# Performance work log

Measured on AMD Instinct MI355X. Metric: run time of the kernel, lower is better.

## Reference

```python
import jax, jax.numpy as jnp
import numpy as np

B, H, S, D = 2, 16, 2048, 64


def setup_inputs() -> dict:
    key = jax.random.key(0)
    kq, kk, kv = jax.random.split(key, 3)
    queries = jax.random.normal(kq, (B, H, S, D), dtype=jnp.float32)
    keys = jax.random.normal(kk, (B, H, S, D), dtype=jnp.float32)
    values = jax.random.normal(kv, (B, H, S, D), dtype=jnp.float32)
    # causal mask: True = attend, False = masked (matches masked_fill(mask == 0, -inf))
    mask = jnp.tril(jnp.ones((S, S), dtype=bool))[None, None, :, :]
    return {"queries": queries, "keys": keys, "values": values, "mask": mask}


def reference(queries, keys, values, mask):
    d_k = queries.shape[-1]
    scale = 1.0 / jnp.sqrt(jnp.asarray(d_k, dtype=queries.dtype))
    # scores: [B,H,S,S]
    scores = jnp.einsum("bhqd,bhkd->bhqk", queries, keys) * scale
    scores = jnp.where(mask, scores, -jnp.inf)
    attention = jax.nn.softmax(scores, axis=-1)
    # dropout p=0.0 (eval-mode reference) -> identity
    return jnp.einsum("bhqk,bhkd->bhqd", attention, values)
```

## Files before the change

kernel.cpp:

```cpp
#include <hip/hip_runtime.h>
#include <hip/hip_bf16.h>

#define S_LEN 2048
#define D_DIM 64
#define KVB   64
#define QS    (0.125f * 1.44269504088896341f)

using f32x4  = __attribute__((ext_vector_type(4))) float;
using bf16x8 = __attribute__((ext_vector_type(8))) short;

__device__ __forceinline__ unsigned short f2bf(float f) {
    return __builtin_bit_cast(unsigned short, __float2bfloat16(f));
}
__device__ __forceinline__ unsigned pk2bf(float lo, float hi) {
    return (unsigned)f2bf(lo) | ((unsigned)f2bf(hi) << 16);
}
__device__ __forceinline__ int swz(int r, int c) {
    return (r * 64 + c) ^ ((r & 7) << 3);
}

template<int C>
__device__ __forceinline__ float dppf(float x) {
    return __builtin_bit_cast(float,
        __builtin_amdgcn_mov_dpp(__builtin_bit_cast(int, x), C, 0xf, 0xf, true));
}
__device__ __forceinline__ float red16_max(float v) {
    v = fmaxf(v, dppf<0xB1>(v));
    v = fmaxf(v, dppf<0x4E>(v));
    v = fmaxf(v, dppf<0x141>(v));
    v = fmaxf(v, dppf<0x140>(v));
    return v;
}
__device__ __forceinline__ float red16_sum(float v) {
    v += dppf<0xB1>(v);
    v += dppf<0x4E>(v);
    v += dppf<0x141>(v);
    v += dppf<0x140>(v);
    return v;
}

typedef const __attribute__((address_space(1))) unsigned short* gas_p;
typedef __attribute__((address_space(3))) unsigned short*       las_p;
__device__ __forceinline__ void stage16(const unsigned short* g, unsigned short* l) {
    __builtin_amdgcn_global_load_lds((gas_p)g, (las_p)l, 16, 0, 0);
}

__global__ __launch_bounds__(256)
void prep_k(const float* __restrict__ Kg, unsigned short* __restrict__ wsK) {
    const int base = (blockIdx.x * 256 + threadIdx.x) * 8;
    const int bh   = base >> 17;
    const int rem  = base & 131071;
    const int r    = rem >> 6;
    const int c0   = rem & 63;
    f32x4 a = *(const f32x4*)(Kg + base);
    f32x4 b = *(const f32x4*)(Kg + base + 4);
    union { uint4 w4; unsigned u[4]; } w;
    w.u[0] = pk2bf(a[0], a[1]); w.u[1] = pk2bf(a[2], a[3]);
    w.u[2] = pk2bf(b[0], b[1]); w.u[3] = pk2bf(b[2], b[3]);
    *(uint4*)&wsK[bh * 131072 + (r >> 6) * 4096 + swz(r & 63, c0)] = w.w4;
}

__global__ __launch_bounds__(256)
void prep_v(const float* __restrict__ Vg, unsigned short* __restrict__ wsV) {
    __shared__ float ldsF[64 * 68];
    const int bh  = blockIdx.x >> 5;
    const int t   = blockIdx.x & 31;
    const int tid = threadIdx.x;
    const int kvr = tid >> 2;
    const int c0  = (tid & 3) << 4;
    const float* src = Vg + (size_t)bh * 131072 + (size_t)(t * 64 + kvr) * 64 + c0;
    #pragma unroll
    for (int j = 0; j < 4; ++j)
        *(f32x4*)&ldsF[kvr * 68 + c0 + j * 4] = *(const f32x4*)(src + j * 4);
    __syncthreads();
    #pragma unroll
    for (int i = 0; i < 2; ++i) {
        const int d   = tid & 63;
        const int kv0 = ((tid >> 6) << 3) + (i << 5);
        float p[8];
        #pragma unroll
        for (int j = 0; j < 8; ++j) p[j] = ldsF[(kv0 + j) * 68 + d];
        union { uint4 w4; unsigned u[4]; } w;
        w.u[0] = pk2bf(p[0], p[1]); w.u[1] = pk2bf(p[2], p[3]);
        w.u[2] = pk2bf(p[4], p[5]); w.u[3] = pk2bf(p[6], p[7]);
        *(uint4*)&wsV[bh * 131072 + t * 4096 + swz(d, kv0)] = w.w4;
    }
}

__global__ __launch_bounds__(256, 4)
void attn_fast(const float* __restrict__ Qg, const unsigned short* __restrict__ wsK,
               const unsigned short* __restrict__ wsV, float* __restrict__ Og) {
    __shared__ __align__(16) unsigned short lds[20480];

    const int wg = blockIdx.x;
    const int x  = wg & 7;
    const int s  = (wg >> 3) & 31;
    const int r  = wg >> 8;
    const int bh = x * 4 + r;
    const int q  = (r & 1) ? (31 - s) : s;

    const int tid  = threadIdx.x;
    const int wid  = tid >> 6;
    const int lane = tid & 63;
    const int lo   = lane & 15;
    const int hi   = lane >> 4;

    const float* Qp = Qg + (size_t)bh * (S_LEN * D_DIM);
    float*       Op = Og + (size_t)bh * (S_LEN * D_DIM);
    const unsigned short* kws = wsK + (size_t)bh * 131072;
    const unsigned short* vws = wsV + (size_t)bh * 131072;

    const int qrow0 = q * 64 + wid * 16;

    bf16x8 qf[2];
    #pragma unroll
    for (int kc = 0; kc < 2; ++kc) {
        const float* src = Qp + (size_t)(qrow0 + lo) * D_DIM + kc * 32 + hi * 8;
        f32x4 a = *(const f32x4*)src;
        f32x4 b = *(const f32x4*)(src + 4);
        union { bf16x8 v; unsigned u[4]; } fr;
        fr.u[0] = pk2bf(a[0] * QS, a[1] * QS);
        fr.u[1] = pk2bf(a[2] * QS, a[3] * QS);
        fr.u[2] = pk2bf(b[0] * QS, b[1] * QS);
        fr.u[3] = pk2bf(b[2] * QS, b[3] * QS);
        qf[kc] = fr.v;
    }

    float mrow[4], lrow[4];
    f32x4 oacc[4];
    #pragma unroll
    for (int rr = 0; rr < 4; ++rr) { mrow[rr] = -INFINITY; lrow[rr] = 0.f; }
    #pragma unroll
    for (int dn = 0; dn < 4; ++dn) oacc[dn] = f32x4{0.f, 0.f, 0.f, 0.f};

    const int pbase = 16384 + (wid << 10);
    const int T = q + 1;

    #pragma unroll
    for (int j = 0; j < 2; ++j) {
        const int so = (wid * 2 + j) * 512;
        stage16(kws + so + lane * 8, &lds[so]);
        stage16(vws + so + lane * 8, &lds[4096 + so]);
    }
    __syncthreads();

    for (int t = 0; t < T; ++t) {
        const int kA = (t & 1) << 13;
        const int vA = kA + 4096;
        const bool pf = (t + 1 < T);

        if (pf) {
            const int nA = ((t + 1) & 1) << 13;
            const int tb = (t + 1) * 4096;
            #pragma unroll
            for (int j = 0; j < 2; ++j) {
                const int so = (wid * 2 + j) * 512;
                stage16(kws + tb + so + lane * 8, &lds[nA + so]);
                stage16(vws + tb + so + lane * 8, &lds[nA + 4096 + so]);
            }
        }

        f32x4 sc[4];
        __builtin_amdgcn_s_setprio(1);
        #pragma unroll
        for (int nt = 0; nt < 4; ++nt) {
            f32x4 acc = f32x4{0.f, 0.f, 0.f, 0.f};
            #pragma unroll
            for (int kc = 0; kc < 2; ++kc) {
                bf16x8 kf = *(const bf16x8*)&lds[kA + swz(nt * 16 + lo, kc * 32 + hi * 8)];
                acc = __builtin_amdgcn_mfma_f32_16x16x32_bf16(qf[kc], kf, acc, 0, 0, 0);
            }
            sc[nt] = acc;
        }
        __builtin_amdgcn_s_setprio(0);
        if (t == q) {
            const int kb = t * KVB;
            #pragma unroll
            for (int nt = 0; nt < 4; ++nt)
                #pragma unroll
                for (int rr = 0; rr < 4; ++rr)
                    if (kb + nt * 16 + lo > qrow0 + hi * 4 + rr) sc[nt][rr] = -INFINITY;
        }
        float pm[4];
        #pragma unroll
        for (int rr = 0; rr < 4; ++rr)
            pm[rr] = red16_max(fmaxf(fmaxf(sc[0][rr], sc[1][rr]), fmaxf(sc[2][rr], sc[3][rr])));

        bool resc = false;
        #pragma unroll
        for (int rr = 0; rr < 4; ++rr) resc |= (pm[rr] > mrow[rr] + 8.f);
        if (__any(resc)) {
            #pragma unroll
            for (int rr = 0; rr < 4; ++rr) {
                const float mn = fmaxf(mrow[rr], pm[rr]);
                const float al = __builtin_amdgcn_exp2f(mrow[rr] - mn);
                mrow[rr] = mn;
                lrow[rr] *= al;
                #pragma unroll
                for (int dn = 0; dn < 4; ++dn) oacc[dn][rr] *= al;
            }
        }
        float rs[4] = {0.f, 0.f, 0.f, 0.f};
        #pragma unroll
        for (int nt = 0; nt < 4; ++nt)
            #pragma unroll
            for (int rr = 0; rr < 4; ++rr) {
                float p = __builtin_amdgcn_exp2f(sc[nt][rr] - mrow[rr]);
                rs[rr] += p;
                lds[pbase + swz(hi * 4 + rr, nt * 16 + lo)] = f2bf(p);
            }
        #pragma unroll
        for (int rr = 0; rr < 4; ++rr) lrow[rr] += red16_sum(rs[rr]);

        __builtin_amdgcn_s_setprio(1);
        #pragma unroll
        for (int dn = 0; dn < 4; ++dn)
            #pragma unroll
            for (int kc = 0; kc < 2; ++kc) {
                bf16x8 pfr = *(const bf16x8*)&lds[pbase + swz(lo, kc * 32 + hi * 8)];
                bf16x8 vfr = *(const bf16x8*)&lds[vA + swz(dn * 16 + lo, kc * 32 + hi * 8)];
                oacc[dn] = __builtin_amdgcn_mfma_f32_16x16x32_bf16(pfr, vfr, oacc[dn], 0, 0, 0);
            }
        __builtin_amdgcn_s_setprio(0);

        __syncthreads();
    }

    #pragma unroll
    for (int rr = 0; rr < 4; ++rr) {
        const float inv = 1.0f / lrow[rr];
        #pragma unroll
        for (int dn = 0; dn < 4; ++dn)
            Op[(size_t)(qrow0 + hi * 4 + rr) * D_DIM + dn * 16 + lo] = oacc[dn][rr] * inv;
    }
}

__global__ __launch_bounds__(256, 4)
void attn_fb(const float* __restrict__ Qg, const float* __restrict__ Kg,
             const float* __restrict__ Vg, float* __restrict__ Og) {
    __shared__ __align__(16) unsigned short lds[20480];
    const int wg = blockIdx.x;
    const int x  = wg & 7;
    const int s  = (wg >> 3) & 31;
    const int r  = wg >> 8;
    const int bh = x * 4 + r;
    const int q  = (r & 1) ? (31 - s) : s;
    const int tid  = threadIdx.x;
    const int wid  = tid >> 6;
    const int lane = tid & 63;
    const int lo   = lane & 15;
    const int hi   = lane >> 4;
    const size_t boff = (size_t)bh * (S_LEN * D_DIM);
    const float* Qp = Qg + boff;
    const float* Kp = Kg + boff;
    const float* Vp = Vg + boff;
    float*       Op = Og + boff;
    const int qrow0 = q * 64 + wid * 16;
    bf16x8 qf[2];
    #pragma unroll
    for (int kc = 0; kc < 2; ++kc) {
        const float* src = Qp + (size_t)(qrow0 + lo) * D_DIM + kc * 32 + hi * 8;
        f32x4 a = *(const f32x4*)src;
        f32x4 b = *(const f32x4*)(src + 4);
        union { bf16x8 v; unsigned u[4]; } fr;
        fr.u[0] = pk2bf(a[0] * QS, a[1] * QS);
        fr.u[1] = pk2bf(a[2] * QS, a[3] * QS);
        fr.u[2] = pk2bf(b[0] * QS, b[1] * QS);
        fr.u[3] = pk2bf(b[2] * QS, b[3] * QS);
        qf[kc] = fr.v;
    }
    float mrow[4], lrow[4];
    f32x4 oacc[4];
    #pragma unroll
    for (int rr = 0; rr < 4; ++rr) { mrow[rr] = -INFINITY; lrow[rr] = 0.f; }
    #pragma unroll
    for (int dn = 0; dn < 4; ++dn) oacc[dn] = f32x4{0.f, 0.f, 0.f, 0.f};
    const int kr    = tid >> 2;
    const int kcb   = (tid & 3) << 4;
    const int vr    = (tid & 31) << 1;
    const int vcb   = (tid >> 5) << 3;
    const int pbase = 16384 + (wid << 10);
    const int T = q + 1;
    f32x4 kst[4], vst[4];
    {
        const float* ks = Kp + (size_t)kr * D_DIM + kcb;
        kst[0] = *(const f32x4*)ks;       kst[1] = *(const f32x4*)(ks + 4);
        kst[2] = *(const f32x4*)(ks + 8); kst[3] = *(const f32x4*)(ks + 12);
        const float* vs = Vp + (size_t)vr * D_DIM + vcb;
        vst[0] = *(const f32x4*)vs;           vst[1] = *(const f32x4*)(vs + 4);
        vst[2] = *(const f32x4*)(vs + D_DIM); vst[3] = *(const f32x4*)(vs + D_DIM + 4);
        union { uint4 w4; unsigned u[4]; } w;
        w.u[0] = pk2bf(kst[0][0], kst[0][1]); w.u[1] = pk2bf(kst[0][2], kst[0][3]);
        w.u[2] = pk2bf(kst[1][0], kst[1][1]); w.u[3] = pk2bf(kst[1][2], kst[1][3]);
        *(uint4*)&lds[swz(kr, kcb)] = w.w4;
        w.u[0] = pk2bf(kst[2][0], kst[2][1]); w.u[1] = pk2bf(kst[2][2], kst[2][3]);
        w.u[2] = pk2bf(kst[3][0], kst[3][1]); w.u[3] = pk2bf(kst[3][2], kst[3][3]);
        *(uint4*)&lds[swz(kr, kcb + 8)] = w.w4;
        #pragma unroll
        for (int c = 0; c < 8; ++c) {
            unsigned pv = pk2bf(vst[c >> 2][c & 3], vst[2 + (c >> 2)][c & 3]);
            *(unsigned*)&lds[4096 + swz(vcb + c, vr)] = pv;
        }
    }
    __syncthreads();
    for (int t = 0; t < T; ++t) {
        const int kA = (t & 1) << 13;
        const int vA = kA + 4096;
        const bool pf = (t + 1 < T);
        if (pf) {
            const int nb = (t + 1) * KVB;
            const float* ks = Kp + (size_t)(nb + kr) * D_DIM + kcb;
            kst[0] = *(const f32x4*)ks;       kst[1] = *(const f32x4*)(ks + 4);
            kst[2] = *(const f32x4*)(ks + 8); kst[3] = *(const f32x4*)(ks + 12);
            const float* vs = Vp + (size_t)(nb + vr) * D_DIM + vcb;
            vst[0] = *(const f32x4*)vs;           vst[1] = *(const f32x4*)(vs + 4);
            vst[2] = *(const f32x4*)(vs + D_DIM); vst[3] = *(const f32x4*)(vs + D_DIM + 4);
        }
        f32x4 sc[4];
        __builtin_amdgcn_s_setprio(1);
        #pragma unroll
        for (int nt = 0; nt < 4; ++nt) {
            f32x4 acc = f32x4{0.f, 0.f, 0.f, 0.f};
            #pragma unroll
            for (int kc = 0; kc < 2; ++kc) {
                bf16x8 kf = *(const bf16x8*)&lds[kA + swz(nt * 16 + lo, kc * 32 + hi * 8)];
                acc = __builtin_amdgcn_mfma_f32_16x16x32_bf16(qf[kc], kf, acc, 0, 0, 0);
            }
            sc[nt] = acc;
        }
        __builtin_amdgcn_s_setprio(0);
        if (t == q) {
            const int kb = t * KVB;
            #pragma unroll
            for (int nt = 0; nt < 4; ++nt)
                #pragma unroll
                for (int rr = 0; rr < 4; ++rr)
                    if (kb + nt * 16 + lo > qrow0 + hi * 4 + rr) sc[nt][rr] = -INFINITY;
        }
        float pm[4];
        #pragma unroll
        for (int rr = 0; rr < 4; ++rr)
            pm[rr] = red16_max(fmaxf(fmaxf(sc[0][rr], sc[1][rr]), fmaxf(sc[2][rr], sc[3][rr])));
        bool resc = false;
        #pragma unroll
        for (int rr = 0; rr < 4; ++rr) resc |= (pm[rr] > mrow[rr] + 8.f);
        if (__any(resc)) {
            #pragma unroll
            for (int rr = 0; rr < 4; ++rr) {
                const float mn = fmaxf(mrow[rr], pm[rr]);
                const float al = __builtin_amdgcn_exp2f(mrow[rr] - mn);
                mrow[rr] = mn;
                lrow[rr] *= al;
                #pragma unroll
                for (int dn = 0; dn < 4; ++dn) oacc[dn][rr] *= al;
            }
        }
        float rs[4] = {0.f, 0.f, 0.f, 0.f};
        #pragma unroll
        for (int nt = 0; nt < 4; ++nt)
            #pragma unroll
            for (int rr = 0; rr < 4; ++rr) {
                float p = __builtin_amdgcn_exp2f(sc[nt][rr] - mrow[rr]);
                rs[rr] += p;
                lds[pbase + swz(hi * 4 + rr, nt * 16 + lo)] = f2bf(p);
            }
        #pragma unroll
        for (int rr = 0; rr < 4; ++rr) lrow[rr] += red16_sum(rs[rr]);
        __builtin_amdgcn_s_setprio(1);
        #pragma unroll
        for (int dn = 0; dn < 4; ++dn)
            #pragma unroll
            for (int kc = 0; kc < 2; ++kc) {
                bf16x8 pfr = *(const bf16x8*)&lds[pbase + swz(lo, kc * 32 + hi * 8)];
                bf16x8 vfr = *(const bf16x8*)&lds[vA + swz(dn * 16 + lo, kc * 32 + hi * 8)];
                oacc[dn] = __builtin_amdgcn_mfma_f32_16x16x32_bf16(pfr, vfr, oacc[dn], 0, 0, 0);
            }
        __builtin_amdgcn_s_setprio(0);
        if (pf) {
            const int nA = ((t + 1) & 1) << 13;
            union { uint4 w4; unsigned u[4]; } w;
            w.u[0] = pk2bf(kst[0][0], kst[0][1]); w.u[1] = pk2bf(kst[0][2], kst[0][3]);
            w.u[2] = pk2bf(kst[1][0], kst[1][1]); w.u[3] = pk2bf(kst[1][2], kst[1][3]);
            *(uint4*)&lds[nA + swz(kr, kcb)] = w.w4;
            w.u[0] = pk2bf(kst[2][0], kst[2][1]); w.u[1] = pk2bf(kst[2][2], kst[2][3]);
            w.u[2] = pk2bf(kst[3][0], kst[3][1]); w.u[3] = pk2bf(kst[3][2], kst[3][3]);
            *(uint4*)&lds[nA + swz(kr, kcb + 8)] = w.w4;
            #pragma unroll
            for (int c = 0; c < 8; ++c) {
                unsigned pv = pk2bf(vst[c >> 2][c & 3], vst[2 + (c >> 2)][c & 3]);
                *(unsigned*)&lds[nA + 4096 + swz(vcb + c, vr)] = pv;
            }
        }
        __syncthreads();
    }
    #pragma unroll
    for (int rr = 0; rr < 4; ++rr) {
        const float inv = 1.0f / lrow[rr];
        #pragma unroll
        for (int dn = 0; dn < 4; ++dn)
            Op[(size_t)(qrow0 + hi * 4 + rr) * D_DIM + dn * 16 + lo] = oacc[dn][rr] * inv;
    }
}

extern "C" void kernel_launch(void* const* d_in, const int* in_sizes, int n_in,
                              void* d_out, int out_size, void* d_ws, size_t ws_size,
                              hipStream_t stream) {
    const float* Q = (const float*)d_in[0];
    const float* K = (const float*)d_in[1];
    const float* V = (const float*)d_in[2];
    float* O = (float*)d_out;
    const size_t wsNeed = (size_t)32 * 131072 * 2 * sizeof(unsigned short);
    if (ws_size >= wsNeed) {
        unsigned short* wsK = (unsigned short*)d_ws;
        unsigned short* wsV = wsK + (size_t)32 * 131072;
        prep_k<<<dim3(2048), dim3(256), 0, stream>>>(K, wsK);
        prep_v<<<dim3(1024), dim3(256), 0, stream>>>(V, wsV);
        attn_fast<<<dim3(1024), dim3(256), 0, stream>>>(Q, wsK, wsV, O);
    } else {
        attn_fb<<<dim3(1024), dim3(256), 0, stream>>>(Q, K, V, O);
    }
}
```

Measured before the change: 151.0 us.

## Split long causal query tiles across two workgroups and merge partials

Query tiles with 16 or more KV tiles are split into two KV halves, each handled by a separate workgroup that writes unnormalized partial outputs plus row max and sum to workspace. A new combine kernel rescales and merges the two halves. This targets the tail imbalance of causal attention, where the longest tiles dominate runtime. The K and V prep kernels are also fused into one launch that writes transposed V through LDS. The cost is extra workspace traffic, a third launch, and a dependence on workspace being large enough.

Result: no change. 149.2 us (-1.2%).

```diff
diff --git a/kernel.cpp b/kernel.cpp
--- a/kernel.cpp
+++ b/kernel.cpp
@@ -46,58 +46,77 @@
 }
 
 __global__ __launch_bounds__(256)
-void prep_k(const float* __restrict__ Kg, unsigned short* __restrict__ wsK) {
-    const int base = (blockIdx.x * 256 + threadIdx.x) * 8;
-    const int bh   = base >> 17;
-    const int rem  = base & 131071;
-    const int r    = rem >> 6;
-    const int c0   = rem & 63;
-    f32x4 a = *(const f32x4*)(Kg + base);
-    f32x4 b = *(const f32x4*)(Kg + base + 4);
-    union { uint4 w4; unsigned u[4]; } w;
-    w.u[0] = pk2bf(a[0], a[1]); w.u[1] = pk2bf(a[2], a[3]);
-    w.u[2] = pk2bf(b[0], b[1]); w.u[3] = pk2bf(b[2], b[3]);
-    *(uint4*)&wsK[bh * 131072 + (r >> 6) * 4096 + swz(r & 63, c0)] = w.w4;
-}
-
-__global__ __launch_bounds__(256)
-void prep_v(const float* __restrict__ Vg, unsigned short* __restrict__ wsV) {
-    __shared__ float ldsF[64 * 68];
+void prep_kv(const float* __restrict__ Kg, const float* __restrict__ Vg,
+             unsigned short* __restrict__ wsK, unsigned short* __restrict__ wsV) {
+    __shared__ float vf[64 * 68];
+    __shared__ __align__(16) unsigned short vt[4096];
     const int bh  = blockIdx.x >> 5;
     const int t   = blockIdx.x & 31;
     const int tid = threadIdx.x;
-    const int kvr = tid >> 2;
-    const int c0  = (tid & 3) << 4;
-    const float* src = Vg + (size_t)bh * 131072 + (size_t)(t * 64 + kvr) * 64 + c0;
-    #pragma unroll
-    for (int j = 0; j < 4; ++j)
-        *(f32x4*)&ldsF[kvr * 68 + c0 + j * 4] = *(const f32x4*)(src + j * 4);
+    const size_t gbase = (size_t)bh * 131072 + (size_t)t * 4096;
+    {
+        const int e  = tid * 16;
+        const int r  = e >> 6;
+        const int c0 = e & 63;
+        const float* src = Kg + gbase + e;
+        f32x4 a = *(const f32x4*)src;
+        f32x4 b = *(const f32x4*)(src + 4);
+        f32x4 cc = *(const f32x4*)(src + 8);
+        f32x4 d = *(const f32x4*)(src + 12);
+        union { uint4 w4; unsigned u[4]; } w;
+        w.u[0] = pk2bf(a[0], a[1]);  w.u[1] = pk2bf(a[2], a[3]);
+        w.u[2] = pk2bf(b[0], b[1]);  w.u[3] = pk2bf(b[2], b[3]);
+        *(uint4*)&wsK[gbase + swz(r, c0)] = w.w4;
+        w.u[0] = pk2bf(cc[0], cc[1]); w.u[1] = pk2bf(cc[2], cc[3]);
+        w.u[2] = pk2bf(d[0], d[1]);   w.u[3] = pk2bf(d[2], d[3]);
+        *(uint4*)&wsK[gbase + swz(r, c0 + 8)] = w.w4;
+        const float* vsrc = Vg + gbase + e;
+        *(f32x4*)&vf[r * 68 + c0]      = *(const f32x4*)vsrc;
+        *(f32x4*)&vf[r * 68 + c0 + 4]  = *(const f32x4*)(vsrc + 4);
+        *(f32x4*)&vf[r * 68 + c0 + 8]  = *(const f32x4*)(vsrc + 8);
+        *(f32x4*)&vf[r * 68 + c0 + 12] = *(const f32x4*)(vsrc + 12);
+    }
     __syncthreads();
-    #pragma unroll
-    for (int i = 0; i < 2; ++i) {
+    {
         const int d   = tid & 63;
-        const int kv0 = ((tid >> 6) << 3) + (i << 5);
-        float p[8];
-        #pragma unroll
-        for (int j = 0; j < 8; ++j) p[j] = ldsF[(kv0 + j) * 68 + d];
+        const int kv0 = (tid >> 6) << 4;
+        float p[16];
+        #pragma unroll
+        for (int j = 0; j < 16; ++j) p[j] = vf[(kv0 + j) * 68 + d];
         union { uint4 w4; unsigned u[4]; } w;
-        w.u[0] = pk2bf(p[0], p[1]); w.u[1] = pk2bf(p[2], p[3]);
-        w.u[2] = pk2bf(p[4], p[5]); w.u[3] = pk2bf(p[6], p[7]);
-        *(uint4*)&wsV[bh * 131072 + t * 4096 + swz(d, kv0)] = w.w4;
+        w.u[0] = pk2bf(p[0], p[1]);   w.u[1] = pk2bf(p[2], p[3]);
+        w.u[2] = pk2bf(p[4], p[5]);   w.u[3] = pk2bf(p[6], p[7]);
+        *(uint4*)&vt[swz(d, kv0)] = w.w4;
+        w.u[0] = pk2bf(p[8], p[9]);   w.u[1] = pk2bf(p[10], p[11]);
+        w.u[2] = pk2bf(p[12], p[13]); w.u[3] = pk2bf(p[14], p[15]);
+        *(uint4*)&vt[swz(d, kv0 + 8)] = w.w4;
+    }
+    __syncthreads();
+    {
+        uint4* dst = (uint4*)&wsV[gbase];
+        const uint4* srcv = (const uint4*)vt;
+        dst[tid] = srcv[tid];
+        dst[tid + 256] = srcv[tid + 256];
     }
 }
 
 __global__ __launch_bounds__(256, 4)
-void attn_fast(const float* __restrict__ Qg, const unsigned short* __restrict__ wsK,
-               const unsigned short* __restrict__ wsV, float* __restrict__ Og) {
+void attn_sp(const float* __restrict__ Qg, const unsigned short* __restrict__ wsK,
+             const unsigned short* __restrict__ wsV, float* __restrict__ Og,
+             float* __restrict__ wsP) {
     __shared__ __align__(16) unsigned short lds[20480];
 
-    const int wg = blockIdx.x;
-    const int x  = wg & 7;
-    const int s  = (wg >> 3) & 31;
-    const int r  = wg >> 8;
-    const int bh = x * 4 + r;
-    const int q  = (r & 1) ? (31 - s) : s;
+    const int blk    = blockIdx.x;
+    const int xcd    = blk & 7;
+    const int within = blk >> 3;
+    const int w      = within >> 2;
+    const int bh     = xcd * 4 + (within & 3);
+    int q, c;
+    if (w < 32) { q = 31 - (w >> 1); c = w & 1; }
+    else        { q = 47 - w;        c = 0;     }
+    const int nc   = (q >= 16) ? 2 : 1;
+    const int t0   = (c == 0) ? 0 : 16;
+    const int tEnd = (c == 0 && q >= 16) ? 16 : (q + 1);
 
     const int tid  = threadIdx.x;
     const int wid  = tid >> 6;
@@ -134,20 +153,22 @@
     for (int dn = 0; dn < 4; ++dn) oacc[dn] = f32x4{0.f, 0.f, 0.f, 0.f};
 
     const int pbase = 16384 + (wid << 10);
-    const int T = q + 1;
-
-    #pragma unroll
-    for (int j = 0; j < 2; ++j) {
-        const int so = (wid * 2 + j) * 512;
-        stage16(kws + so + lane * 8, &lds[so]);
-        stage16(vws + so + lane * 8, &lds[4096 + so]);
+
+    {
+        const int tb = t0 * 4096;
+        #pragma unroll
+        for (int j = 0; j < 2; ++j) {
+            const int so = (wid * 2 + j) * 512;
+            stage16(kws + tb + so + lane * 8, &lds[so]);
+            stage16(vws + tb + so + lane * 8, &lds[4096 + so]);
+        }
     }
     __syncthreads();
 
-    for (int t = 0; t < T; ++t) {
+    for (int t = t0; t < tEnd; ++t) {
         const int kA = (t & 1) << 13;
         const int vA = kA + 4096;
-        const bool pf = (t + 1 < T);
+        const bool pf = (t + 1 < tEnd);
 
         if (pf) {
             const int nA = ((t + 1) & 1) << 13;
@@ -226,6 +247,186 @@
         __syncthreads();
     }
 
+    if (nc == 1) {
+        #pragma unroll
+        for (int rr = 0; rr < 4; ++rr) {
+            const float inv = 1.0f / lrow[rr];
+            #pragma unroll
+            for (int dn = 0; dn < 4; ++dn)
+                Op[(size_t)(qrow0 + hi * 4 + rr) * D_DIM + dn * 16 + lo] = oacc[dn][rr] * inv;
+        }
+    } else {
+        float* slot = wsP + (size_t)(bh * 32 + (q - 16) * 2 + c) * 4224;
+        #pragma unroll
+        for (int rr = 0; rr < 4; ++rr) {
+            const int row = wid * 16 + hi * 4 + rr;
+            #pragma unroll
+            for (int dn = 0; dn < 4; ++dn)
+                slot[row * 64 + dn * 16 + lo] = oacc[dn][rr];
+        }
+        if (lo == 0) {
+            #pragma unroll
+            for (int rr = 0; rr < 4; ++rr) {
+                const int row = wid * 16 + hi * 4 + rr;
+                slot[4096 + row] = mrow[rr];
+                slot[4160 + row] = lrow[rr];
+            }
+        }
+    }
+}
+
+__global__ __launch_bounds__(256)
+void combine_k(const float* __restrict__ wsP, float* __restrict__ Og) {
+    const int bh  = blockIdx.x >> 4;
+    const int qq  = blockIdx.x & 15;
+    const int q   = 16 + qq;
+    const int tid = threadIdx.x;
+    const int row = tid >> 2;
+    const int cg  = (tid & 3) << 4;
+    const float* s0 = wsP + (size_t)(bh * 32 + qq * 2) * 4224;
+    const float* s1 = s0 + 4224;
+    const float m0 = s0[4096 + row], l0 = s0[4160 + row];
+    const float m1 = s1[4096 + row], l1 = s1[4160 + row];
+    const float M  = fmaxf(m0, m1);
+    const float w0 = __builtin_amdgcn_exp2f(m0 - M);
+    const float w1 = __builtin_amdgcn_exp2f(m1 - M);
+    const float inv = 1.0f / (w0 * l0 + w1 * l1);
+    float* dst = Og + (size_t)bh * 131072 + (size_t)(q * 64 + row) * 64 + cg;
+    #pragma unroll
+    for (int j = 0; j < 16; j += 4) {
+        f32x4 a = *(const f32x4*)(s0 + row * 64 + cg + j);
+        f32x4 b = *(const f32x4*)(s1 + row * 64 + cg + j);
+        f32x4 o;
+        #pragma unroll
+        for (int e = 0; e < 4; ++e) o[e] = (w0 * a[e] + w1 * b[e]) * inv;
+        *(f32x4*)(dst + j) = o;
+    }
+}
+
+__global__ __launch_bounds__(256, 4)
+void attn_fast(const float* __restrict__ Qg, const unsigned short* __restrict__ wsK,
+               const unsigned short* __restrict__ wsV, float* __restrict__ Og) {
+    __shared__ __align__(16) unsigned short lds[20480];
+    const int wg = blockIdx.x;
+    const int x  = wg & 7;
+    const int s  = (wg >> 3) & 31;
+    const int r  = wg >> 8;
+    const int bh = x * 4 + r;
+    const int q  = (r & 1) ? (31 - s) : s;
+    const int tid  = threadIdx.x;
+    const int wid  = tid >> 6;
+    const int lane = tid & 63;
+    const int lo   = lane & 15;
+    const int hi   = lane >> 4;
+    const float* Qp = Qg + (size_t)bh * (S_LEN * D_DIM);
+    float*       Op = Og + (size_t)bh * (S_LEN * D_DIM);
+    const unsigned short* kws = wsK + (size_t)bh * 131072;
+    const unsigned short* vws = wsV + (size_t)bh * 131072;
+    const int qrow0 = q * 64 + wid * 16;
+    bf16x8 qf[2];
+    #pragma unroll
+    for (int kc = 0; kc < 2; ++kc) {
+        const float* src = Qp + (size_t)(qrow0 + lo) * D_DIM + kc * 32 + hi * 8;
+        f32x4 a = *(const f32x4*)src;
+        f32x4 b = *(const f32x4*)(src + 4);
+        union { bf16x8 v; unsigned u[4]; } fr;
+        fr.u[0] = pk2bf(a[0] * QS, a[1] * QS);
+        fr.u[1] = pk2bf(a[2] * QS, a[3] * QS);
+        fr.u[2] = pk2bf(b[0] * QS, b[1] * QS);
+        fr.u[3] = pk2bf(b[2] * QS, b[3] * QS);
+        qf[kc] = fr.v;
+    }
+    float mrow[4], lrow[4];
+    f32x4 oacc[4];
+    #pragma unroll
+    for (int rr = 0; rr < 4; ++rr) { mrow[rr] = -INFINITY; lrow[rr] = 0.f; }
+    #pragma unroll
+    for (int dn = 0; dn < 4; ++dn) oacc[dn] = f32x4{0.f, 0.f, 0.f, 0.f};
+    const int pbase = 16384 + (wid << 10);
+    const int T = q + 1;
+    #pragma unroll
+    for (int j = 0; j < 2; ++j) {
+        const int so = (wid * 2 + j) * 512;
+        stage16(kws + so + lane * 8, &lds[so]);
+        stage16(vws + so + lane * 8, &lds[4096 + so]);
+    }
+    __syncthreads();
+    for (int t = 0; t < T; ++t) {
+        const int kA = (t & 1) << 13;
+        const int vA = kA + 4096;
+        const bool pf = (t + 1 < T);
+        if (pf) {
+            const int nA = ((t + 1) & 1) << 13;
+            const int tb = (t + 1) * 4096;
+            #pragma unroll
+            for (int j = 0; j < 2; ++j) {
+                const int so = (wid * 2 + j) * 512;
+                stage16(kws + tb + so + lane * 8, &lds[nA + so]);
+                stage16(vws + tb + so + lane * 8, &lds[nA + 4096 + so]);
+            }
+        }
+        f32x4 sc[4];
+        __builtin_amdgcn_s_setprio(1);
+        #pragma unroll
+        for (int nt = 0; nt < 4; ++nt) {
+            f32x4 acc = f32x4{0.f, 0.f, 0.f, 0.f};
+            #pragma unroll
+            for (int kc = 0; kc < 2; ++kc) {
+                bf16x8 kf = *(const bf16x8*)&lds[kA + swz(nt * 16 + lo, kc * 32 + hi * 8)];
+                acc = __builtin_amdgcn_mfma_f32_16x16x32_bf16(qf[kc], kf, acc, 0, 0, 0);
+            }
+            sc[nt] = acc;
+        }
+        __builtin_amdgcn_s_setprio(0);
+        if (t == q) {
+            const int kb = t * KVB;
+            #pragma unroll
+            for (int nt = 0; nt < 4; ++nt)
+                #pragma unroll
+                for (int rr = 0; rr < 4; ++rr)
+                    if (kb + nt * 16 + lo > qrow0 + hi * 4 + rr) sc[nt][rr] = -INFINITY;
+        }
+        float pm[4];
+        #pragma unroll
+        for (int rr = 0; rr < 4; ++rr)
+            pm[rr] = red16_max(fmaxf(fmaxf(sc[0][rr], sc[1][rr]), fmaxf(sc[2][rr], sc[3][rr])));
+        bool resc = false;
+        #pragma unroll
+        for (int rr = 0; rr < 4; ++rr) resc |= (pm[rr] > mrow[rr] + 8.f);
+        if (__any(resc)) {
+            #pragma unroll
+            for (int rr = 0; rr < 4; ++rr) {
+                const float mn = fmaxf(mrow[rr], pm[rr]);
+                const float al = __builtin_amdgcn_exp2f(mrow[rr] - mn);
+                mrow[rr] = mn;
+                lrow[rr] *= al;
+                #pragma unroll
+                for (int dn = 0; dn < 4; ++dn) oacc[dn][rr] *= al;
+            }
+        }
+        float rs[4] = {0.f, 0.f, 0.f, 0.f};
+        #pragma unroll
+        for (int nt = 0; nt < 4; ++nt)
+            #pragma unroll
+            for (int rr = 0; rr < 4; ++rr) {
+                float p = __builtin_amdgcn_exp2f(sc[nt][rr] - mrow[rr]);
+                rs[rr] += p;
+                lds[pbase + swz(hi * 4 + rr, nt * 16 + lo)] = f2bf(p);
+            }
+        #pragma unroll
+        for (int rr = 0; rr < 4; ++rr) lrow[rr] += red16_sum(rs[rr]);
+        __builtin_amdgcn_s_setprio(1);
+        #pragma unroll
+        for (int dn = 0; dn < 4; ++dn)
+            #pragma unroll
+            for (int kc = 0; kc < 2; ++kc) {
+                bf16x8 pfr = *(const bf16x8*)&lds[pbase + swz(lo, kc * 32 + hi * 8)];
+                bf16x8 vfr = *(const bf16x8*)&lds[vA + swz(dn * 16 + lo, kc * 32 + hi * 8)];
+                oacc[dn] = __builtin_amdgcn_mfma_f32_16x16x32_bf16(pfr, vfr, oacc[dn], 0, 0, 0);
+            }
+        __builtin_amdgcn_s_setprio(0);
+        __syncthreads();
+    }
     #pragma unroll
     for (int rr = 0; rr < 4; ++rr) {
         const float inv = 1.0f / lrow[rr];
@@ -297,9 +498,9 @@
         w.u[2] = pk2bf(kst[3][0], kst[3][1]); w.u[3] = pk2bf(kst[3][2], kst[3][3]);
         *(uint4*)&lds[swz(kr, kcb + 8)] = w.w4;
         #pragma unroll
-        for (int c = 0; c < 8; ++c) {
-            unsigned pv = pk2bf(vst[c >> 2][c & 3], vst[2 + (c >> 2)][c & 3]);
-            *(unsigned*)&lds[4096 + swz(vcb + c, vr)] = pv;
+        for (int cc = 0; cc < 8; ++cc) {
+            unsigned pv = pk2bf(vst[cc >> 2][cc & 3], vst[2 + (cc >> 2)][cc & 3]);
+            *(unsigned*)&lds[4096 + swz(vcb + cc, vr)] = pv;
         }
     }
     __syncthreads();
@@ -386,9 +587,9 @@
             w.u[2] = pk2bf(kst[3][0], kst[3][1]); w.u[3] = pk2bf(kst[3][2], kst[3][3]);
             *(uint4*)&lds[nA + swz(kr, kcb + 8)] = w.w4;
             #pragma unroll
-            for (int c = 0; c < 8; ++c) {
-                unsigned pv = pk2bf(vst[c >> 2][c & 3], vst[2 + (c >> 2)][c & 3]);
-                *(unsigned*)&lds[nA + 4096 + swz(vcb + c, vr)] = pv;
+            for (int cc = 0; cc < 8; ++cc) {
+                unsigned pv = pk2bf(vst[cc >> 2][cc & 3], vst[2 + (cc >> 2)][cc & 3]);
+                *(unsigned*)&lds[nA + 4096 + swz(vcb + cc, vr)] = pv;
             }
         }
         __syncthreads();
@@ -409,12 +610,17 @@
     const float* K = (const float*)d_in[1];
     const float* V = (const float*)d_in[2];
     float* O = (float*)d_out;
-    const size_t wsNeed = (size_t)32 * 131072 * 2 * sizeof(unsigned short);
-    if (ws_size >= wsNeed) {
-        unsigned short* wsK = (unsigned short*)d_ws;
-        unsigned short* wsV = wsK + (size_t)32 * 131072;
-        prep_k<<<dim3(2048), dim3(256), 0, stream>>>(K, wsK);
-        prep_v<<<dim3(1024), dim3(256), 0, stream>>>(V, wsV);
+    const size_t prepBytes  = (size_t)32 * 131072 * 2 * sizeof(unsigned short);
+    const size_t splitBytes = prepBytes + (size_t)1024 * 4224 * sizeof(float);
+    unsigned short* wsK = (unsigned short*)d_ws;
+    unsigned short* wsV = wsK + (size_t)32 * 131072;
+    float*          wsP = (float*)(wsV + (size_t)32 * 131072);
+    if (ws_size >= splitBytes) {
+        prep_kv<<<dim3(1024), dim3(256), 0, stream>>>(K, V, wsK, wsV);
+        attn_sp<<<dim3(1536), dim3(256), 0, stream>>>(Q, wsK, wsV, O, wsP);
+        combine_k<<<dim3(512), dim3(256), 0, stream>>>(wsP, O);
+    } else if (ws_size >= prepBytes) {
+        prep_kv<<<dim3(1024), dim3(256), 0, stream>>>(K, V, wsK, wsV);
         attn_fast<<<dim3(1024), dim3(256), 0, stream>>>(Q, wsK, wsV, O);
     } else {
         attn_fb<<<dim3(1024), dim3(256), 0, stream>>>(Q, K, V, O);
```
